# Performance work log

Measured on AMD Instinct MI355X. Metric: run time of the kernel, lower is better.

The kernel has to match this reference:

```python
import jax, jax.numpy as jnp
import numpy as np
from jax.ops import segment_sum

N = 100000   # nodes
E = 1600000  # edges
F = 128      # node feature dim
H = 128      # hidden dim
FE = 16      # edge feature dim
G = 256      # num graphs
EPS = 1e-5   # batch-norm eps


def setup_inputs() -> dict:
    key = jax.random.key(0)
    ks = jax.random.split(key, 16)
    s = 0.05
    return {
        "x": jax.random.normal(ks[0], (N, F), jnp.float32),
        "edge_index": jax.random.randint(ks[1], (2, E), 0, N, dtype=jnp.int32),
        "edge_attr": jax.random.normal(ks[2], (E, FE), jnp.float32),
        "batch_idx": jnp.sort(jax.random.randint(ks[3], (N,), 0, G, dtype=jnp.int32)),
        # GCN layer 1
        "W_g1": jax.random.normal(ks[4], (F, H), jnp.float32) * s,
        "b_g1": jnp.zeros((H,), jnp.float32),
        "gamma1": jnp.ones((H,), jnp.float32),
        "beta1": jnp.zeros((H,), jnp.float32),
        # GCN layer 2
        "W_g2": jax.random.normal(ks[5], (H, H), jnp.float32) * s,
        "b_g2": jnp.zeros((H,), jnp.float32),
        "gamma2": jnp.ones((H,), jnp.float32),
        "beta2": jnp.zeros((H,), jnp.float32),
        # edge encoder MLP
        "W_e1": jax.random.normal(ks[6], (FE, H), jnp.float32) * s,
        "b_e1": jnp.zeros((H,), jnp.float32),
        "W_e2": jax.random.normal(ks[7], (H, H), jnp.float32) * s,
        "b_e2": jnp.zeros((H,), jnp.float32),
    }


def _gcn_bn_relu(x, src, dst, W, b, gamma, beta):
    """GCNConv (sym-normalized, self-loops) + BatchNorm1d (batch stats) + ReLU."""
    h = x @ W                                             # [N, H]
    ones = jnp.ones((E,), h.dtype)
    deg = segment_sum(ones, dst, num_segments=N) + 1.0    # self-loop degree
    dinv = jax.lax.rsqrt(deg)                             # [N]
    norm = dinv[src] * dinv[dst]                          # [E]
    agg = segment_sum(h[src] * norm[:, None], dst, num_segments=N)
    out = agg + h * (dinv * dinv)[:, None] + b            # self-loop + bias
    mu = out.mean(axis=0)
    var = out.var(axis=0)
    out = (out - mu) * jax.lax.rsqrt(var + EPS) * gamma + beta
    return jax.nn.relu(out)


def reference(x, edge_index, edge_attr, batch_idx, W_g1, b_g1, gamma1, beta1,
              W_g2, b_g2, gamma2, beta2, W_e1, b_e1, W_e2, b_e2):
    src, dst = edge_index[0], edge_index[1]
    h = _gcn_bn_relu(x, src, dst, W_g1, b_g1, gamma1, beta1)
    h = _gcn_bn_relu(h, src, dst, W_g2, b_g2, gamma2, beta2)

    # global mean pool over nodes per graph
    node_cnt = segment_sum(jnp.ones((N,), h.dtype), batch_idx, num_segments=G)
    graph_repr = segment_sum(h, batch_idx, num_segments=G) / jnp.maximum(node_cnt, 1.0)[:, None]

    # edge encoder MLP + per-graph edge mean (vectorized version of the loop)
    e = jax.nn.relu(edge_attr @ W_e1 + b_e1) @ W_e2 + b_e2   # [E, H]
    edge_batch = batch_idx[src]                              # [E]
    edge_cnt = segment_sum(jnp.ones((E,), e.dtype), edge_batch, num_segments=G)
    edge_sum = segment_sum(e, edge_batch, num_segments=G)
    edge_repr = jnp.where(edge_cnt[:, None] > 0, edge_sum / jnp.maximum(edge_cnt, 1.0)[:, None], 0.0)

    return graph_repr + edge_repr  # [G, H]
```

## Files before the change

### kernel.cpp

```cpp
#include <hip/hip_runtime.h>
#include <cstdint>

__device__ inline unsigned int bfpack2(float a, float b) {
  unsigned int ua = __float_as_uint(a), ub = __float_as_uint(b);
  ua += 0x7FFFu + ((ua >> 16) & 1u);
  ub += 0x7FFFu + ((ub >> 16) & 1u);
  return (ua >> 16) | (ub & 0xFFFF0000u);
}
__device__ inline float bflo(unsigned int u) { return __uint_as_float(u << 16); }
__device__ inline float bfhi(unsigned int u) { return __uint_as_float(u & 0xFFFF0000u); }

__global__ __launch_bounds__(256) void pre_kernel(const int* __restrict__ src,
                                                  const int* __restrict__ dst,
                                                  int* __restrict__ deg,
                                                  int* __restrict__ deg2, int nE) {
  int e = blockIdx.x * 256 + threadIdx.x;
  if (e < nE) {
    atomicAdd(&deg[dst[e]], 1);
    atomicAdd(&deg2[src[e]], 1);
  }
}

__global__ __launch_bounds__(256) void dinv_kernel(const int* __restrict__ deg,
                                                   float* __restrict__ dinv, int n) {
  int i = blockIdx.x * 256 + threadIdx.x;
  if (i < n) dinv[i] = rsqrtf((float)deg[i] + 1.0f);
}

__global__ __launch_bounds__(256) void scan1_kernel(const int* __restrict__ deg,
                                                    int* __restrict__ rp,
                                                    int* __restrict__ part, int n, int pad) {
  __shared__ int sh[256];
  int b = blockIdx.x, t = threadIdx.x;
  int base = b * 1024 + t * 4;
  int v0 = (base + 0 < n) ? deg[base + 0] : 0;
  int v1 = (base + 1 < n) ? deg[base + 1] : 0;
  int v2 = (base + 2 < n) ? deg[base + 2] : 0;
  int v3 = (base + 3 < n) ? deg[base + 3] : 0;
  if (pad) {
    v0 = (v0 + 7) & ~7; v1 = (v1 + 7) & ~7;
    v2 = (v2 + 7) & ~7; v3 = (v3 + 7) & ~7;
  }
  int ts = v0 + v1 + v2 + v3;
  sh[t] = ts;
  __syncthreads();
  for (int off = 1; off < 256; off <<= 1) {
    int x = (t >= off) ? sh[t - off] : 0;
    __syncthreads();
    sh[t] += x;
    __syncthreads();
  }
  int excl = sh[t] - ts;
  if (t == 255) part[b] = sh[255];
  if (base + 0 < n) rp[base + 0] = excl;
  if (base + 1 < n) rp[base + 1] = excl + v0;
  if (base + 2 < n) rp[base + 2] = excl + v0 + v1;
  if (base + 3 < n) rp[base + 3] = excl + v0 + v1 + v2;
}

__global__ void scan2_kernel(int* part, int* rp, int nb, int n) {
  if (blockIdx.x == 0 && threadIdx.x == 0) {
    int run = 0;
    for (int i = 0; i < nb; ++i) { int v = part[i]; part[i] = run; run += v; }
    rp[n] = run;
  }
}

__global__ __launch_bounds__(256) void scan3_kernel(int* __restrict__ rp,
                                                    const int* __restrict__ part,
                                                    int* __restrict__ cursor, int n) {
  int i = blockIdx.x * 256 + threadIdx.x;
  if (i < n) {
    int v = rp[i] + part[i >> 10];
    rp[i] = v;
    cursor[i] = v;
  }
}

__global__ __launch_bounds__(256) void place_kernel(const int* __restrict__ src,
                                                    const int* __restrict__ dst,
                                                    const int* __restrict__ batch,
                                                    const float* __restrict__ dinv,
                                                    int* __restrict__ cursor,
                                                    int* __restrict__ cursor2,
                                                    int* __restrict__ ssort,
                                                    float* __restrict__ wgtv,
                                                    unsigned int* __restrict__ epk, int nE) {
  int e = blockIdx.x * 256 + threadIdx.x;
  if (e < nE) {
    int s = src[e];
    int d = dst[e];
    int p1 = atomicAdd(&cursor[d], 1);
    ssort[p1] = s;
    wgtv[p1] = dinv[s] * dinv[d];
    int g = batch[s];
    int p2 = atomicAdd(&cursor2[s], 1);
    epk[p2] = ((unsigned int)g << 21) | (unsigned int)e;
  }
}

__global__ __launch_bounds__(256) void pad_kernel(const int* __restrict__ rp,
                                                  const int* __restrict__ deg,
                                                  int* __restrict__ ssort,
                                                  float* __restrict__ wgtv, int nN) {
  int i = blockIdx.x * 256 + threadIdx.x;
  if (i < nN) {
    int b = rp[i] + deg[i], e = rp[i + 1];
    for (int k = b; k < e; ++k) { ssort[k] = i; wgtv[k] = 0.f; }
  }
}

template <bool FUSED>
__global__ __launch_bounds__(256) void gemm128_kernel(const float* __restrict__ A,
                                                      const float* __restrict__ W,
                                                      const float* __restrict__ scale,
                                                      const float* __restrict__ shift,
                                                      unsigned int* __restrict__ hpk,
                                                      int nrows) {
  extern __shared__ float lds[];
  float* Ws = lds;
  float* xs = lds + 128 * 128;
  const int t = threadIdx.x;
  for (int i = t; i < (128 * 128) / 4; i += 256)
    reinterpret_cast<float4*>(Ws)[i] = reinterpret_cast<const float4*>(W)[i];
  const int wave = t >> 6, lane = t & 63;
  for (int rb = blockIdx.x * 16; rb < nrows; rb += gridDim.x * 16) {
    int nr = min(16, nrows - rb);
    __syncthreads();
    for (int i = t; i < nr * 32; i += 256) {
      float4 v = reinterpret_cast<const float4*>(A + (size_t)rb * 128)[i];
      if (FUSED) {
        float4 sc4 = reinterpret_cast<const float4*>(scale)[i & 31];
        float4 sh4 = reinterpret_cast<const float4*>(shift)[i & 31];
        v.x = fmaxf(fmaf(v.x, sc4.x, sh4.x), 0.f);
        v.y = fmaxf(fmaf(v.y, sc4.y, sh4.y), 0.f);
        v.z = fmaxf(fmaf(v.z, sc4.z, sh4.z), 0.f);
        v.w = fmaxf(fmaf(v.w, sc4.w, sh4.w), 0.f);
      }
      reinterpret_cast<float4*>(xs)[i] = v;
    }
    __syncthreads();
    float acc[4][2] = {{0.f, 0.f}, {0.f, 0.f}, {0.f, 0.f}, {0.f, 0.f}};
    const float* xw = xs + wave * 4 * 128;
#pragma unroll 4
    for (int k = 0; k < 128; ++k) {
      float w0 = Ws[k * 128 + lane];
      float w1 = Ws[k * 128 + 64 + lane];
#pragma unroll
      for (int r = 0; r < 4; ++r) {
        float a = xw[r * 128 + k];
        acc[r][0] = fmaf(a, w0, acc[r][0]);
        acc[r][1] = fmaf(a, w1, acc[r][1]);
      }
    }
#pragma unroll
    for (int r = 0; r < 4; ++r) {
      int row = rb + wave * 4 + r;
      if (row < nrows)
        hpk[(size_t)row * 64 + lane] = bfpack2(acc[r][0], acc[r][1]);
    }
  }
}

__global__ __launch_bounds__(256) void spmm_kernel(const unsigned int* __restrict__ hpk,
                                                   const float* __restrict__ dinv,
                                                   const int* __restrict__ rp,
                                                   const int* __restrict__ srcs,
                                                   const float* __restrict__ wgtv,
                                                   const float* __restrict__ bias,
                                                   float* __restrict__ outp,
                                                   float* __restrict__ bnsum,
                                                   float* __restrict__ bnsq, int nN) {
  const int lane = threadIdx.x & 63;
  const int wid = (blockIdx.x * blockDim.x + threadIdx.x) >> 6;
  const int nw = (gridDim.x * blockDim.x) >> 6;
  float b0 = bias[lane], b1 = bias[64 + lane];
  float s0 = 0.f, s1 = 0.f, q0 = 0.f, q1 = 0.f;
  for (int n = wid; n < nN; n += nw) {
    const int beg = rp[n], end = rp[n + 1];
    float aA0 = 0.f, aA1 = 0.f, aB0 = 0.f, aB1 = 0.f;
    for (int j = beg; j < end; j += 8) {
      int4 ia = reinterpret_cast<const int4*>(srcs + j)[0];
      int4 ib = reinterpret_cast<const int4*>(srcs + j)[1];
      float4 wa = reinterpret_cast<const float4*>(wgtv + j)[0];
      float4 wb = reinterpret_cast<const float4*>(wgtv + j)[1];
      unsigned int p0 = hpk[(size_t)ia.x * 64 + lane];
      unsigned int p1 = hpk[(size_t)ia.y * 64 + lane];
      unsigned int p2 = hpk[(size_t)ia.z * 64 + lane];
      unsigned int p3 = hpk[(size_t)ia.w * 64 + lane];
      unsigned int p4 = hpk[(size_t)ib.x * 64 + lane];
      unsigned int p5 = hpk[(size_t)ib.y * 64 + lane];
      unsigned int p6 = hpk[(size_t)ib.z * 64 + lane];
      unsigned int p7 = hpk[(size_t)ib.w * 64 + lane];
      aA0 = fmaf(wa.x, bflo(p0), aA0); aA1 = fmaf(wa.x, bfhi(p0), aA1);
      aB0 = fmaf(wa.y, bflo(p1), aB0); aB1 = fmaf(wa.y, bfhi(p1), aB1);
      aA0 = fmaf(wa.z, bflo(p2), aA0); aA1 = fmaf(wa.z, bfhi(p2), aA1);
      aB0 = fmaf(wa.w, bflo(p3), aB0); aB1 = fmaf(wa.w, bfhi(p3), aB1);
      aA0 = fmaf(wb.x, bflo(p4), aA0); aA1 = fmaf(wb.x, bfhi(p4), aA1);
      aB0 = fmaf(wb.y, bflo(p5), aB0); aB1 = fmaf(wb.y, bfhi(p5), aB1);
      aA0 = fmaf(wb.z, bflo(p6), aA0); aA1 = fmaf(wb.z, bfhi(p6), aA1);
      aB0 = fmaf(wb.w, bflo(p7), aB0); aB1 = fmaf(wb.w, bfhi(p7), aB1);
    }
    float a0 = aA0 + aB0, a1 = aA1 + aB1;
    float dn = dinv[n];
    float sw = dn * dn;
    unsigned int pn = hpk[(size_t)n * 64 + lane];
    float o0 = fmaf(bflo(pn), sw, a0) + b0;
    float o1 = fmaf(bfhi(pn), sw, a1) + b1;
    outp[(size_t)n * 128 + lane] = o0;
    outp[(size_t)n * 128 + 64 + lane] = o1;
    s0 += o0; s1 += o1;
    q0 = fmaf(o0, o0, q0); q1 = fmaf(o1, o1, q1);
  }
  atomicAdd(&bnsum[lane], s0);
  atomicAdd(&bnsum[64 + lane], s1);
  atomicAdd(&bnsq[lane], q0);
  atomicAdd(&bnsq[64 + lane], q1);
}

__global__ void bnfin_kernel(const float* __restrict__ sum, const float* __restrict__ sq,
                             const float* __restrict__ gamma, const float* __restrict__ beta,
                             float* __restrict__ scale, float* __restrict__ shift,
                             float invN) {
  int c = threadIdx.x;
  float mu = sum[c] * invN;
  float var = sq[c] * invN - mu * mu;
  float sc = gamma[c] * rsqrtf(var + 1e-5f);
  scale[c] = sc;
  shift[c] = beta[c] - mu * sc;
}

__global__ __launch_bounds__(256) void pool_kernel(const float* __restrict__ h,
                                                   const int* __restrict__ batch,
                                                   const float* __restrict__ scale,
                                                   const float* __restrict__ shift,
                                                   float* __restrict__ gsum,
                                                   float* __restrict__ gcnt,
                                                   int nN, int chunk) {
  const int lane = threadIdx.x & 63;
  const int wid = (blockIdx.x * blockDim.x + threadIdx.x) >> 6;
  int beg = wid * chunk;
  if (beg >= nN) return;
  int end = min(nN, beg + chunk);
  const int c2 = 2 * lane;
  float2 sc2 = *reinterpret_cast<const float2*>(scale + c2);
  float2 sh2 = *reinterpret_cast<const float2*>(shift + c2);
  int cur = -1;
  float a0 = 0.f, a1 = 0.f, cnt = 0.f;
  for (int n = beg; n < end; ++n) {
    int g = batch[n];
    if (g != cur) {
      if (cur >= 0) {
        atomicAdd(&gsum[cur * 128 + c2], a0);
        atomicAdd(&gsum[cur * 128 + c2 + 1], a1);
        if (lane == 0) atomicAdd(&gcnt[cur], cnt);
      }
      cur = g; a0 = 0.f; a1 = 0.f; cnt = 0.f;
    }
    float2 v = *reinterpret_cast<const float2*>(h + (size_t)n * 128 + c2);
    a0 += fmaxf(fmaf(v.x, sc2.x, sh2.x), 0.f);
    a1 += fmaxf(fmaf(v.y, sc2.y, sh2.y), 0.f);
    cnt += 1.f;
  }
  if (cur >= 0) {
    atomicAdd(&gsum[cur * 128 + c2], a0);
    atomicAdd(&gsum[cur * 128 + c2 + 1], a1);
    if (lane == 0) atomicAdd(&gcnt[cur], cnt);
  }
}

__global__ __launch_bounds__(256) void edge2_kernel(const float* __restrict__ ea,
                                                    const unsigned int* __restrict__ epk,
                                                    const float* __restrict__ We1,
                                                    const float* __restrict__ be1,
                                                    float* __restrict__ esum,
                                                    float* __restrict__ ecnt,
                                                    int nE, int chunk) {
  const int lane = threadIdx.x & 63;
  const int wid = (blockIdx.x * blockDim.x + threadIdx.x) >> 6;
  int beg = wid * chunk;
  if (beg >= nE) return;
  int end = min(nE, beg + chunk);
  float w0[16], w1[16];
#pragma unroll
  for (int k = 0; k < 16; ++k) {
    w0[k] = We1[k * 128 + lane];
    w1[k] = We1[k * 128 + 64 + lane];
  }
  float b0 = be1[lane], b1 = be1[64 + lane];
  int cur = -1;
  float a0 = 0.f, a1 = 0.f, cnt = 0.f;
  for (int j = beg; j < end; ++j) {
    unsigned int pk = epk[j];
    int g = (int)(pk >> 21);
    int e = (int)(pk & 0x1FFFFFu);
    if (g != cur) {
      if (cur >= 0) {
        atomicAdd(&esum[cur * 128 + lane], a0);
        atomicAdd(&esum[cur * 128 + 64 + lane], a1);
        if (lane == 0) atomicAdd(&ecnt[cur], cnt);
      }
      cur = g; a0 = 0.f; a1 = 0.f; cnt = 0.f;
    }
    const float4* eap = reinterpret_cast<const float4*>(ea + (size_t)e * 16);
    float4 t0 = eap[0], t1 = eap[1], t2 = eap[2], t3 = eap[3];
    float u0 = b0, u1 = b1;
    u0 = fmaf(t0.x, w0[0], u0);  u1 = fmaf(t0.x, w1[0], u1);
    u0 = fmaf(t0.y, w0[1], u0);  u1 = fmaf(t0.y, w1[1], u1);
    u0 = fmaf(t0.z, w0[2], u0);  u1 = fmaf(t0.z, w1[2], u1);
    u0 = fmaf(t0.w, w0[3], u0);  u1 = fmaf(t0.w, w1[3], u1);
    u0 = fmaf(t1.x, w0[4], u0);  u1 = fmaf(t1.x, w1[4], u1);
    u0 = fmaf(t1.y, w0[5], u0);  u1 = fmaf(t1.y, w1[5], u1);
    u0 = fmaf(t1.z, w0[6], u0);  u1 = fmaf(t1.z, w1[6], u1);
    u0 = fmaf(t1.w, w0[7], u0);  u1 = fmaf(t1.w, w1[7], u1);
    u0 = fmaf(t2.x, w0[8], u0);  u1 = fmaf(t2.x, w1[8], u1);
    u0 = fmaf(t2.y, w0[9], u0);  u1 = fmaf(t2.y, w1[9], u1);
    u0 = fmaf(t2.z, w0[10], u0); u1 = fmaf(t2.z, w1[10], u1);
    u0 = fmaf(t2.w, w0[11], u0); u1 = fmaf(t2.w, w1[11], u1);
    u0 = fmaf(t3.x, w0[12], u0); u1 = fmaf(t3.x, w1[12], u1);
    u0 = fmaf(t3.y, w0[13], u0); u1 = fmaf(t3.y, w1[13], u1);
    u0 = fmaf(t3.z, w0[14], u0); u1 = fmaf(t3.z, w1[14], u1);
    u0 = fmaf(t3.w, w0[15], u0); u1 = fmaf(t3.w, w1[15], u1);
    a0 += fmaxf(u0, 0.f);
    a1 += fmaxf(u1, 0.f);
    cnt += 1.f;
  }
  if (cur >= 0) {
    atomicAdd(&esum[cur * 128 + lane], a0);
    atomicAdd(&esum[cur * 128 + 64 + lane], a1);
    if (lane == 0) atomicAdd(&ecnt[cur], cnt);
  }
}

__global__ __launch_bounds__(128) void final_kernel(const float* __restrict__ gsum,
                                                    const float* __restrict__ gcnt,
                                                    const float* __restrict__ esum,
                                                    const float* __restrict__ ecnt,
                                                    const float* __restrict__ We2,
                                                    const float* __restrict__ be2,
                                                    float* __restrict__ out) {
  __shared__ float row[128];
  int g = blockIdx.x, c = threadIdx.x;
  row[c] = esum[g * 128 + c];
  __syncthreads();
  float acc = 0.f;
#pragma unroll 4
  for (int k = 0; k < 128; ++k) acc = fmaf(row[k], We2[k * 128 + c], acc);
  float ce = ecnt[g];
  float er = (ce > 0.f) ? (acc / ce + be2[c]) : 0.f;
  float cn = gcnt[g];
  float gr = gsum[g * 128 + c] / fmaxf(cn, 1.f);
  out[g * 128 + c] = gr + er;
}

extern "C" void kernel_launch(void* const* d_in, const int* in_sizes, int n_in,
                              void* d_out, int out_size, void* d_ws, size_t ws_size,
                              hipStream_t stream) {
  const float* x    = (const float*)d_in[0];
  const int*   ei   = (const int*)d_in[1];
  const float* ea   = (const float*)d_in[2];
  const int*   bidx = (const int*)d_in[3];
  const float* Wg1  = (const float*)d_in[4];
  const float* bg1  = (const float*)d_in[5];
  const float* gm1  = (const float*)d_in[6];
  const float* bt1  = (const float*)d_in[7];
  const float* Wg2  = (const float*)d_in[8];
  const float* bg2  = (const float*)d_in[9];
  const float* gm2  = (const float*)d_in[10];
  const float* bt2  = (const float*)d_in[11];
  const float* We1  = (const float*)d_in[12];
  const float* be1  = (const float*)d_in[13];
  const float* We2  = (const float*)d_in[14];
  const float* be2  = (const float*)d_in[15];
  float* out = (float*)d_out;

  const int N = in_sizes[3];
  const int E = in_sizes[1] / 2;
  const int G = out_size / 128;
  const int* srcp = ei;
  const int* dstp = ei + E;
  const int Epad = E + 8 * N;

  char* w = (char*)d_ws;
  auto alloc = [&](size_t b) {
    char* p = w;
    w += (b + 15) & ~(size_t)15;
    return p;
  };
  float* bufB    = (float*)alloc((size_t)N * 128 * 4);
  unsigned int* hpk = (unsigned int*)alloc((size_t)N * 64 * 4);
  int*   ssort   = (int*)alloc((size_t)Epad * 4);
  float* wgtv    = (float*)alloc((size_t)Epad * 4);
  unsigned int* epk = (unsigned int*)alloc((size_t)E * 4);
  int*   rp      = (int*)alloc((size_t)(N + 1) * 4);
  int*   rp2     = (int*)alloc((size_t)(N + 1) * 4);
  int*   cursor  = (int*)alloc((size_t)N * 4);
  int*   cursor2 = (int*)alloc((size_t)N * 4);
  float* dinv    = (float*)alloc((size_t)N * 4);
  char* zbase = w;
  int*   deg  = (int*)alloc((size_t)N * 4);
  int*   deg2 = (int*)alloc((size_t)N * 4);
  float* bs1  = (float*)alloc(512);
  float* bq1  = (float*)alloc(512);
  float* bs2  = (float*)alloc(512);
  float* bq2  = (float*)alloc(512);
  float* gsum = (float*)alloc((size_t)G * 128 * 4);
  float* gcnt = (float*)alloc((size_t)G * 4);
  float* esum = (float*)alloc((size_t)G * 128 * 4);
  float* ecnt = (float*)alloc((size_t)G * 4);
  int*   part  = (int*)alloc(4096);
  int*   part2 = (int*)alloc(4096);
  size_t zbytes = (size_t)(w - zbase);
  float* sc1 = (float*)alloc(512);
  float* sh1 = (float*)alloc(512);
  float* sc2 = (float*)alloc(512);
  float* sh2 = (float*)alloc(512);

  hipMemsetAsync(zbase, 0, zbytes, stream);

  (void)hipFuncSetAttribute((const void*)gemm128_kernel<false>,
                            hipFuncAttributeMaxDynamicSharedMemorySize, 73728);
  (void)hipFuncSetAttribute((const void*)gemm128_kernel<true>,
                            hipFuncAttributeMaxDynamicSharedMemorySize, 73728);

  pre_kernel<<<(E + 255) / 256, 256, 0, stream>>>(srcp, dstp, deg, deg2, E);
  dinv_kernel<<<(N + 255) / 256, 256, 0, stream>>>(deg, dinv, N);
  int nb = (N + 1023) / 1024;
  scan1_kernel<<<nb, 256, 0, stream>>>(deg, rp, part, N, 1);
  scan2_kernel<<<1, 1, 0, stream>>>(part, rp, nb, N);
  scan3_kernel<<<(N + 255) / 256, 256, 0, stream>>>(rp, part, cursor, N);
  scan1_kernel<<<nb, 256, 0, stream>>>(deg2, rp2, part2, N, 0);
  scan2_kernel<<<1, 1, 0, stream>>>(part2, rp2, nb, N);
  scan3_kernel<<<(N + 255) / 256, 256, 0, stream>>>(rp2, part2, cursor2, N);
  place_kernel<<<(E + 255) / 256, 256, 0, stream>>>(srcp, dstp, bidx, dinv, cursor,
                                                    cursor2, ssort, wgtv, epk, E);
  pad_kernel<<<(N + 255) / 256, 256, 0, stream>>>(rp, deg, ssort, wgtv, N);

  gemm128_kernel<false><<<512, 256, 73728, stream>>>(x, Wg1, nullptr, nullptr, hpk, N);
  spmm_kernel<<<2048, 256, 0, stream>>>(hpk, dinv, rp, ssort, wgtv, bg1, bufB, bs1, bq1, N);
  bnfin_kernel<<<1, 128, 0, stream>>>(bs1, bq1, gm1, bt1, sc1, sh1, 1.0f / (float)N);

  gemm128_kernel<true><<<512, 256, 73728, stream>>>(bufB, Wg2, sc1, sh1, hpk, N);
  spmm_kernel<<<2048, 256, 0, stream>>>(hpk, dinv, rp, ssort, wgtv, bg2, bufB, bs2, bq2, N);
  bnfin_kernel<<<1, 128, 0, stream>>>(bs2, bq2, gm2, bt2, sc2, sh2, 1.0f / (float)N);

  int nwp = (2048 * 256) / 64;
  int chunkN = (N + nwp - 1) / nwp;
  pool_kernel<<<2048, 256, 0, stream>>>(bufB, bidx, sc2, sh2, gsum, gcnt, N, chunkN);
  int nwe = (2048 * 256) / 64;
  int chunkE = (E + nwe - 1) / nwe;
  edge2_kernel<<<2048, 256, 0, stream>>>(ea, epk, We1, be1, esum, ecnt, E, chunkE);
  final_kernel<<<G, 128, 0, stream>>>(gsum, gcnt, esum, ecnt, We2, be2, out);
}
```

Before: 1.527 ms.

## Merge preprocessing launches, interleave CSR index/weight, co-run edge MLP with SpMM

Collapses the two scan pipelines and the dinv computation into three combined launches, and merges placement with padding into one kernel, which cuts the number of small launches. The CSR source index and normalization weight are now stored interleaved as int2, so SpMM reads both with one stream of vector loads instead of two separate arrays. The edge-encoder reduction is moved into extra blocks of the first SpMM launch so it runs alongside the memory-bound aggregation rather than as its own pass. The trade-off is that edge blocks now compete with SpMM for compute units and bandwidth, and the edge work is split across fewer waves with larger chunks.

```diff
diff --git a/kernel.cpp b/kernel.cpp
--- a/kernel.cpp
+++ b/kernel.cpp
@@ -21,22 +21,25 @@
   }
 }
 
-__global__ __launch_bounds__(256) void dinv_kernel(const int* __restrict__ deg,
-                                                   float* __restrict__ dinv, int n) {
-  int i = blockIdx.x * 256 + threadIdx.x;
-  if (i < n) dinv[i] = rsqrtf((float)deg[i] + 1.0f);
-}
-
-__global__ __launch_bounds__(256) void scan1_kernel(const int* __restrict__ deg,
+__global__ __launch_bounds__(256) void scanA_kernel(const int* __restrict__ deg,
+                                                    const int* __restrict__ deg2,
                                                     int* __restrict__ rp,
-                                                    int* __restrict__ part, int n, int pad) {
+                                                    int* __restrict__ rp2,
+                                                    int* __restrict__ part,
+                                                    int* __restrict__ part2,
+                                                    int n, int nb) {
   __shared__ int sh[256];
   int b = blockIdx.x, t = threadIdx.x;
-  int base = b * 1024 + t * 4;
-  int v0 = (base + 0 < n) ? deg[base + 0] : 0;
-  int v1 = (base + 1 < n) ? deg[base + 1] : 0;
-  int v2 = (base + 2 < n) ? deg[base + 2] : 0;
-  int v3 = (base + 3 < n) ? deg[base + 3] : 0;
+  const int* d = (b < nb) ? deg : deg2;
+  int* r = (b < nb) ? rp : rp2;
+  int* p = (b < nb) ? part : part2;
+  int pad = (b < nb) ? 1 : 0;
+  int bb = (b < nb) ? b : b - nb;
+  int base = bb * 1024 + t * 4;
+  int v0 = (base + 0 < n) ? d[base + 0] : 0;
+  int v1 = (base + 1 < n) ? d[base + 1] : 0;
+  int v2 = (base + 2 < n) ? d[base + 2] : 0;
+  int v3 = (base + 3 < n) ? d[base + 3] : 0;
   if (pad) {
     v0 = (v0 + 7) & ~7; v1 = (v1 + 7) & ~7;
     v2 = (v2 + 7) & ~7; v3 = (v3 + 7) & ~7;
@@ -51,62 +54,71 @@
     __syncthreads();
   }
   int excl = sh[t] - ts;
-  if (t == 255) part[b] = sh[255];
-  if (base + 0 < n) rp[base + 0] = excl;
-  if (base + 1 < n) rp[base + 1] = excl + v0;
-  if (base + 2 < n) rp[base + 2] = excl + v0 + v1;
-  if (base + 3 < n) rp[base + 3] = excl + v0 + v1 + v2;
-}
-
-__global__ void scan2_kernel(int* part, int* rp, int nb, int n) {
-  if (blockIdx.x == 0 && threadIdx.x == 0) {
+  if (t == 255) p[bb] = sh[255];
+  if (base + 0 < n) r[base + 0] = excl;
+  if (base + 1 < n) r[base + 1] = excl + v0;
+  if (base + 2 < n) r[base + 2] = excl + v0 + v1;
+  if (base + 3 < n) r[base + 3] = excl + v0 + v1 + v2;
+}
+
+__global__ void scanB_kernel(int* part, int* part2, int* rp, int* rp2, int nb, int n) {
+  if (threadIdx.x == 0) {
+    int* p = (blockIdx.x == 0) ? part : part2;
+    int* r = (blockIdx.x == 0) ? rp : rp2;
     int run = 0;
-    for (int i = 0; i < nb; ++i) { int v = part[i]; part[i] = run; run += v; }
-    rp[n] = run;
-  }
-}
-
-__global__ __launch_bounds__(256) void scan3_kernel(int* __restrict__ rp,
+    for (int i = 0; i < nb; ++i) { int v = p[i]; p[i] = run; run += v; }
+    r[n] = run;
+  }
+}
+
+__global__ __launch_bounds__(256) void scanC_kernel(int* __restrict__ rp,
+                                                    int* __restrict__ rp2,
                                                     const int* __restrict__ part,
-                                                    int* __restrict__ cursor, int n) {
+                                                    const int* __restrict__ part2,
+                                                    int* __restrict__ cursor,
+                                                    int* __restrict__ cursor2,
+                                                    const int* __restrict__ deg,
+                                                    float* __restrict__ dinv, int n) {
   int i = blockIdx.x * 256 + threadIdx.x;
   if (i < n) {
     int v = rp[i] + part[i >> 10];
     rp[i] = v;
     cursor[i] = v;
-  }
-}
-
-__global__ __launch_bounds__(256) void place_kernel(const int* __restrict__ src,
-                                                    const int* __restrict__ dst,
-                                                    const int* __restrict__ batch,
-                                                    const float* __restrict__ dinv,
-                                                    int* __restrict__ cursor,
-                                                    int* __restrict__ cursor2,
-                                                    int* __restrict__ ssort,
-                                                    float* __restrict__ wgtv,
-                                                    unsigned int* __restrict__ epk, int nE) {
-  int e = blockIdx.x * 256 + threadIdx.x;
-  if (e < nE) {
-    int s = src[e];
-    int d = dst[e];
+    dinv[i] = rsqrtf((float)deg[i] + 1.0f);
+  } else if (i < 2 * n) {
+    int j = i - n;
+    int v = rp2[j] + part2[j >> 10];
+    rp2[j] = v;
+    cursor2[j] = v;
+  }
+}
+
+__global__ __launch_bounds__(256) void placepad_kernel(const int* __restrict__ src,
+                                                       const int* __restrict__ dst,
+                                                       const int* __restrict__ batch,
+                                                       const float* __restrict__ dinv,
+                                                       int* __restrict__ cursor,
+                                                       int* __restrict__ cursor2,
+                                                       int2* __restrict__ swv,
+                                                       unsigned int* __restrict__ epk,
+                                                       const int* __restrict__ rp,
+                                                       const int* __restrict__ deg,
+                                                       int nE, int nN) {
+  int t = blockIdx.x * 256 + threadIdx.x;
+  if (t < nE) {
+    int s = src[t];
+    int d = dst[t];
     int p1 = atomicAdd(&cursor[d], 1);
-    ssort[p1] = s;
-    wgtv[p1] = dinv[s] * dinv[d];
+    int2 sw; sw.x = s; sw.y = __float_as_int(dinv[s] * dinv[d]);
+    swv[p1] = sw;
     int g = batch[s];
     int p2 = atomicAdd(&cursor2[s], 1);
-    epk[p2] = ((unsigned int)g << 21) | (unsigned int)e;
-  }
-}
-
-__global__ __launch_bounds__(256) void pad_kernel(const int* __restrict__ rp,
-                                                  const int* __restrict__ deg,
-                                                  int* __restrict__ ssort,
-                                                  float* __restrict__ wgtv, int nN) {
-  int i = blockIdx.x * 256 + threadIdx.x;
-  if (i < nN) {
+    epk[p2] = ((unsigned int)g << 21) | (unsigned int)t;
+  } else if (t < nE + nN) {
+    int i = t - nE;
     int b = rp[i] + deg[i], e = rp[i + 1];
-    for (int k = b; k < e; ++k) { ssort[k] = i; wgtv[k] = 0.f; }
+    int2 z; z.x = i; z.y = 0;
+    for (int k = b; k < e; ++k) swv[k] = z;
   }
 }
 
@@ -162,44 +174,108 @@
   }
 }
 
-__global__ __launch_bounds__(256) void spmm_kernel(const unsigned int* __restrict__ hpk,
-                                                   const float* __restrict__ dinv,
-                                                   const int* __restrict__ rp,
-                                                   const int* __restrict__ srcs,
-                                                   const float* __restrict__ wgtv,
-                                                   const float* __restrict__ bias,
-                                                   float* __restrict__ outp,
-                                                   float* __restrict__ bnsum,
-                                                   float* __restrict__ bnsq, int nN) {
+__device__ __forceinline__ void edge_body(const float* __restrict__ ea,
+                                          const unsigned int* __restrict__ epk,
+                                          const float* __restrict__ We1,
+                                          const float* __restrict__ be1,
+                                          float* __restrict__ esum,
+                                          float* __restrict__ ecnt,
+                                          int nE, int chunk) {
   const int lane = threadIdx.x & 63;
-  const int wid = (blockIdx.x * blockDim.x + threadIdx.x) >> 6;
-  const int nw = (gridDim.x * blockDim.x) >> 6;
+  const int wid = (blockIdx.x * 256 + threadIdx.x) >> 6;
+  int beg = wid * chunk;
+  if (beg >= nE) return;
+  int end = min(nE, beg + chunk);
+  float w0[16], w1[16];
+#pragma unroll
+  for (int k = 0; k < 16; ++k) {
+    w0[k] = We1[k * 128 + lane];
+    w1[k] = We1[k * 128 + 64 + lane];
+  }
+  float b0 = be1[lane], b1 = be1[64 + lane];
+  int cur = -1;
+  float a0 = 0.f, a1 = 0.f, cnt = 0.f;
+  for (int j = beg; j < end; ++j) {
+    unsigned int pk = epk[j];
+    int g = (int)(pk >> 21);
+    int e = (int)(pk & 0x1FFFFFu);
+    if (g != cur) {
+      if (cur >= 0) {
+        atomicAdd(&esum[cur * 128 + lane], a0);
+        atomicAdd(&esum[cur * 128 + 64 + lane], a1);
+        if (lane == 0) atomicAdd(&ecnt[cur], cnt);
+      }
+      cur = g; a0 = 0.f; a1 = 0.f; cnt = 0.f;
+    }
+    const float4* eap = reinterpret_cast<const float4*>(ea + (size_t)e * 16);
+    float4 t0 = eap[0], t1 = eap[1], t2 = eap[2], t3 = eap[3];
+    float u0 = b0, u1 = b1;
+    u0 = fmaf(t0.x, w0[0], u0);  u1 = fmaf(t0.x, w1[0], u1);
+    u0 = fmaf(t0.y, w0[1], u0);  u1 = fmaf(t0.y, w1[1], u1);
+    u0 = fmaf(t0.z, w0[2], u0);  u1 = fmaf(t0.z, w1[2], u1);
+    u0 = fmaf(t0.w, w0[3], u0);  u1 = fmaf(t0.w, w1[3], u1);
+    u0 = fmaf(t1.x, w0[4], u0);  u1 = fmaf(t1.x, w1[4], u1);
+    u0 = fmaf(t1.y, w0[5], u0);  u1 = fmaf(t1.y, w1[5], u1);
+    u0 = fmaf(t1.z, w0[6], u0);  u1 = fmaf(t1.z, w1[6], u1);
+    u0 = fmaf(t1.w, w0[7], u0);  u1 = fmaf(t1.w, w1[7], u1);
+    u0 = fmaf(t2.x, w0[8], u0);  u1 = fmaf(t2.x, w1[8], u1);
+    u0 = fmaf(t2.y, w0[9], u0);  u1 = fmaf(t2.y, w1[9], u1);
+    u0 = fmaf(t2.z, w0[10], u0); u1 = fmaf(t2.z, w1[10], u1);
+    u0 = fmaf(t2.w, w0[11], u0); u1 = fmaf(t2.w, w1[11], u1);
+    u0 = fmaf(t3.x, w0[12], u0); u1 = fmaf(t3.x, w1[12], u1);
+    u0 = fmaf(t3.y, w0[13], u0); u1 = fmaf(t3.y, w1[13], u1);
+    u0 = fmaf(t3.z, w0[14], u0); u1 = fmaf(t3.z, w1[14], u1);
+    u0 = fmaf(t3.w, w0[15], u0); u1 = fmaf(t3.w, w1[15], u1);
+    a0 += fmaxf(u0, 0.f);
+    a1 += fmaxf(u1, 0.f);
+    cnt += 1.f;
+  }
+  if (cur >= 0) {
+    atomicAdd(&esum[cur * 128 + lane], a0);
+    atomicAdd(&esum[cur * 128 + 64 + lane], a1);
+    if (lane == 0) atomicAdd(&ecnt[cur], cnt);
+  }
+}
+
+__device__ __forceinline__ void spmm_body(const unsigned int* __restrict__ hpk,
+                                          const float* __restrict__ dinv,
+                                          const int* __restrict__ rp,
+                                          const int2* __restrict__ swv,
+                                          const float* __restrict__ bias,
+                                          float* __restrict__ outp,
+                                          float* __restrict__ bnsum,
+                                          float* __restrict__ bnsq, int nN, int eb) {
+  const int lane = threadIdx.x & 63;
+  const int wid = ((blockIdx.x - eb) * 256 + threadIdx.x) >> 6;
+  const int nw = (gridDim.x - eb) * 4;
   float b0 = bias[lane], b1 = bias[64 + lane];
   float s0 = 0.f, s1 = 0.f, q0 = 0.f, q1 = 0.f;
   for (int n = wid; n < nN; n += nw) {
     const int beg = rp[n], end = rp[n + 1];
     float aA0 = 0.f, aA1 = 0.f, aB0 = 0.f, aB1 = 0.f;
     for (int j = beg; j < end; j += 8) {
-      int4 ia = reinterpret_cast<const int4*>(srcs + j)[0];
-      int4 ib = reinterpret_cast<const int4*>(srcs + j)[1];
-      float4 wa = reinterpret_cast<const float4*>(wgtv + j)[0];
-      float4 wb = reinterpret_cast<const float4*>(wgtv + j)[1];
-      unsigned int p0 = hpk[(size_t)ia.x * 64 + lane];
-      unsigned int p1 = hpk[(size_t)ia.y * 64 + lane];
-      unsigned int p2 = hpk[(size_t)ia.z * 64 + lane];
-      unsigned int p3 = hpk[(size_t)ia.w * 64 + lane];
-      unsigned int p4 = hpk[(size_t)ib.x * 64 + lane];
-      unsigned int p5 = hpk[(size_t)ib.y * 64 + lane];
-      unsigned int p6 = hpk[(size_t)ib.z * 64 + lane];
-      unsigned int p7 = hpk[(size_t)ib.w * 64 + lane];
-      aA0 = fmaf(wa.x, bflo(p0), aA0); aA1 = fmaf(wa.x, bfhi(p0), aA1);
-      aB0 = fmaf(wa.y, bflo(p1), aB0); aB1 = fmaf(wa.y, bfhi(p1), aB1);
-      aA0 = fmaf(wa.z, bflo(p2), aA0); aA1 = fmaf(wa.z, bfhi(p2), aA1);
-      aB0 = fmaf(wa.w, bflo(p3), aB0); aB1 = fmaf(wa.w, bfhi(p3), aB1);
-      aA0 = fmaf(wb.x, bflo(p4), aA0); aA1 = fmaf(wb.x, bfhi(p4), aA1);
-      aB0 = fmaf(wb.y, bflo(p5), aB0); aB1 = fmaf(wb.y, bfhi(p5), aB1);
-      aA0 = fmaf(wb.z, bflo(p6), aA0); aA1 = fmaf(wb.z, bfhi(p6), aA1);
-      aB0 = fmaf(wb.w, bflo(p7), aB0); aB1 = fmaf(wb.w, bfhi(p7), aB1);
+      const int4* q = reinterpret_cast<const int4*>(swv + j);
+      int4 A = q[0], B = q[1], C = q[2], D = q[3];
+      unsigned int p0 = hpk[(size_t)A.x * 64 + lane];
+      unsigned int p1 = hpk[(size_t)A.z * 64 + lane];
+      unsigned int p2 = hpk[(size_t)B.x * 64 + lane];
+      unsigned int p3 = hpk[(size_t)B.z * 64 + lane];
+      unsigned int p4 = hpk[(size_t)C.x * 64 + lane];
+      unsigned int p5 = hpk[(size_t)C.z * 64 + lane];
+      unsigned int p6 = hpk[(size_t)D.x * 64 + lane];
+      unsigned int p7 = hpk[(size_t)D.z * 64 + lane];
+      float w0 = __int_as_float(A.y), w1 = __int_as_float(A.w);
+      float w2 = __int_as_float(B.y), w3 = __int_as_float(B.w);
+      float w4 = __int_as_float(C.y), w5 = __int_as_float(C.w);
+      float w6 = __int_as_float(D.y), w7 = __int_as_float(D.w);
+      aA0 = fmaf(w0, bflo(p0), aA0); aA1 = fmaf(w0, bfhi(p0), aA1);
+      aB0 = fmaf(w1, bflo(p1), aB0); aB1 = fmaf(w1, bfhi(p1), aB1);
+      aA0 = fmaf(w2, bflo(p2), aA0); aA1 = fmaf(w2, bfhi(p2), aA1);
+      aB0 = fmaf(w3, bflo(p3), aB0); aB1 = fmaf(w3, bfhi(p3), aB1);
+      aA0 = fmaf(w4, bflo(p4), aA0); aA1 = fmaf(w4, bfhi(p4), aA1);
+      aB0 = fmaf(w5, bflo(p5), aB0); aB1 = fmaf(w5, bfhi(p5), aB1);
+      aA0 = fmaf(w6, bflo(p6), aA0); aA1 = fmaf(w6, bfhi(p6), aA1);
+      aB0 = fmaf(w7, bflo(p7), aB0); aB1 = fmaf(w7, bfhi(p7), aB1);
     }
     float a0 = aA0 + aB0, a1 = aA1 + aB1;
     float dn = dinv[n];
@@ -216,6 +292,28 @@
   atomicAdd(&bnsum[64 + lane], s1);
   atomicAdd(&bnsq[lane], q0);
   atomicAdd(&bnsq[64 + lane], q1);
+}
+
+__global__ __launch_bounds__(256) void spmm_edge_kernel(const unsigned int* __restrict__ hpk,
+                                                        const float* __restrict__ dinv,
+                                                        const int* __restrict__ rp,
+                                                        const int2* __restrict__ swv,
+                                                        const float* __restrict__ bias,
+                                                        float* __restrict__ outp,
+                                                        float* __restrict__ bnsum,
+                                                        float* __restrict__ bnsq, int nN,
+                                                        const float* __restrict__ ea,
+                                                        const unsigned int* __restrict__ epk,
+                                                        const float* __restrict__ We1,
+                                                        const float* __restrict__ be1,
+                                                        float* __restrict__ esum,
+                                                        float* __restrict__ ecnt,
+                                                        int nE, int chunkE, int eb) {
+  if ((int)blockIdx.x < eb) {
+    edge_body(ea, epk, We1, be1, esum, ecnt, nE, chunkE);
+  } else {
+    spmm_body(hpk, dinv, rp, swv, bias, outp, bnsum, bnsq, nN, eb);
+  }
 }
 
 __global__ void bnfin_kernel(const float* __restrict__ sum, const float* __restrict__ sq,
@@ -269,69 +367,6 @@
   }
 }
 
-__global__ __launch_bounds__(256) void edge2_kernel(const float* __restrict__ ea,
-                                                    const unsigned int* __restrict__ epk,
-                                                    const float* __restrict__ We1,
-                                                    const float* __restrict__ be1,
-                                                    float* __restrict__ esum,
-                                                    float* __restrict__ ecnt,
-                                                    int nE, int chunk) {
-  const int lane = threadIdx.x & 63;
-  const int wid = (blockIdx.x * blockDim.x + threadIdx.x) >> 6;
-  int beg = wid * chunk;
-  if (beg >= nE) return;
-  int end = min(nE, beg + chunk);
-  float w0[16], w1[16];
-#pragma unroll
-  for (int k = 0; k < 16; ++k) {
-    w0[k] = We1[k * 128 + lane];
-    w1[k] = We1[k * 128 + 64 + lane];
-  }
-  float b0 = be1[lane], b1 = be1[64 + lane];
-  int cur = -1;
-  float a0 = 0.f, a1 = 0.f, cnt = 0.f;
-  for (int j = beg; j < end; ++j) {
-    unsigned int pk = epk[j];
-    int g = (int)(pk >> 21);
-    int e = (int)(pk & 0x1FFFFFu);
-    if (g != cur) {
-      if (cur >= 0) {
-        atomicAdd(&esum[cur * 128 + lane], a0);
-        atomicAdd(&esum[cur * 128 + 64 + lane], a1);
-        if (lane == 0) atomicAdd(&ecnt[cur], cnt);
-      }
-      cur = g; a0 = 0.f; a1 = 0.f; cnt = 0.f;
-    }
-    const float4* eap = reinterpret_cast<const float4*>(ea + (size_t)e * 16);
-    float4 t0 = eap[0], t1 = eap[1], t2 = eap[2], t3 = eap[3];
-    float u0 = b0, u1 = b1;
-    u0 = fmaf(t0.x, w0[0], u0);  u1 = fmaf(t0.x, w1[0], u1);
-    u0 = fmaf(t0.y, w0[1], u0);  u1 = fmaf(t0.y, w1[1], u1);
-    u0 = fmaf(t0.z, w0[2], u0);  u1 = fmaf(t0.z, w1[2], u1);
-    u0 = fmaf(t0.w, w0[3], u0);  u1 = fmaf(t0.w, w1[3], u1);
-    u0 = fmaf(t1.x, w0[4], u0);  u1 = fmaf(t1.x, w1[4], u1);
-    u0 = fmaf(t1.y, w0[5], u0);  u1 = fmaf(t1.y, w1[5], u1);
-    u0 = fmaf(t1.z, w0[6], u0);  u1 = fmaf(t1.z, w1[6], u1);
-    u0 = fmaf(t1.w, w0[7], u0);  u1 = fmaf(t1.w, w1[7], u1);
-    u0 = fmaf(t2.x, w0[8], u0);  u1 = fmaf(t2.x, w1[8], u1);
-    u0 = fmaf(t2.y, w0[9], u0);  u1 = fmaf(t2.y, w1[9], u1);
-    u0 = fmaf(t2.z, w0[10], u0); u1 = fmaf(t2.z, w1[10], u1);
-    u0 = fmaf(t2.w, w0[11], u0); u1 = fmaf(t2.w, w1[11], u1);
-    u0 = fmaf(t3.x, w0[12], u0); u1 = fmaf(t3.x, w1[12], u1);
-    u0 = fmaf(t3.y, w0[13], u0); u1 = fmaf(t3.y, w1[13], u1);
-    u0 = fmaf(t3.z, w0[14], u0); u1 = fmaf(t3.z, w1[14], u1);
-    u0 = fmaf(t3.w, w0[15], u0); u1 = fmaf(t3.w, w1[15], u1);
-    a0 += fmaxf(u0, 0.f);
-    a1 += fmaxf(u1, 0.f);
-    cnt += 1.f;
-  }
-  if (cur >= 0) {
-    atomicAdd(&esum[cur * 128 + lane], a0);
-    atomicAdd(&esum[cur * 128 + 64 + lane], a1);
-    if (lane == 0) atomicAdd(&ecnt[cur], cnt);
-  }
-}
-
 __global__ __launch_bounds__(128) void final_kernel(const float* __restrict__ gsum,
                                                     const float* __restrict__ gcnt,
                                                     const float* __restrict__ esum,
@@ -389,8 +424,7 @@
   };
   float* bufB    = (float*)alloc((size_t)N * 128 * 4);
   unsigned int* hpk = (unsigned int*)alloc((size_t)N * 64 * 4);
-  int*   ssort   = (int*)alloc((size_t)Epad * 4);
-  float* wgtv    = (float*)alloc((size_t)Epad * 4);
+  int2*  swv     = (int2*)alloc((size_t)Epad * 8);
   unsigned int* epk = (unsigned int*)alloc((size_t)E * 4);
   int*   rp      = (int*)alloc((size_t)(N + 1) * 4);
   int*   rp2     = (int*)alloc((size_t)(N + 1) * 4);
@@ -424,31 +458,30 @@
                             hipFuncAttributeMaxDynamicSharedMemorySize, 73728);
 
   pre_kernel<<<(E + 255) / 256, 256, 0, stream>>>(srcp, dstp, deg, deg2, E);
-  dinv_kernel<<<(N + 255) / 256, 256, 0, stream>>>(deg, dinv, N);
   int nb = (N + 1023) / 1024;
-  scan1_kernel<<<nb, 256, 0, stream>>>(deg, rp, part, N, 1);
-  scan2_kernel<<<1, 1, 0, stream>>>(part, rp, nb, N);
-  scan3_kernel<<<(N + 255) / 256, 256, 0, stream>>>(rp, part, cursor, N);
-  scan1_kernel<<<nb, 256, 0, stream>>>(deg2, rp2, part2, N, 0);
-  scan2_kernel<<<1, 1, 0, stream>>>(part2, rp2, nb, N);
-  scan3_kernel<<<(N + 255) / 256, 256, 0, stream>>>(rp2, part2, cursor2, N);
-  place_kernel<<<(E + 255) / 256, 256, 0, stream>>>(srcp, dstp, bidx, dinv, cursor,
-                                                    cursor2, ssort, wgtv, epk, E);
-  pad_kernel<<<(N + 255) / 256, 256, 0, stream>>>(rp, deg, ssort, wgtv, N);
+  scanA_kernel<<<2 * nb, 256, 0, stream>>>(deg, deg2, rp, rp2, part, part2, N, nb);
+  scanB_kernel<<<2, 64, 0, stream>>>(part, part2, rp, rp2, nb, N);
+  scanC_kernel<<<(2 * N + 255) / 256, 256, 0, stream>>>(rp, rp2, part, part2, cursor,
+                                                        cursor2, deg, dinv, N);
+  placepad_kernel<<<(E + N + 255) / 256, 256, 0, stream>>>(srcp, dstp, bidx, dinv, cursor,
+                                                           cursor2, swv, epk, rp, deg, E, N);
+
+  const int EB = 512;
+  int nwe = EB * 4;
+  int chunkE = (E + nwe - 1) / nwe;
 
   gemm128_kernel<false><<<512, 256, 73728, stream>>>(x, Wg1, nullptr, nullptr, hpk, N);
-  spmm_kernel<<<2048, 256, 0, stream>>>(hpk, dinv, rp, ssort, wgtv, bg1, bufB, bs1, bq1, N);
+  spmm_edge_kernel<<<EB + 2048, 256, 0, stream>>>(hpk, dinv, rp, swv, bg1, bufB, bs1, bq1, N,
+                                                  ea, epk, We1, be1, esum, ecnt, E, chunkE, EB);
   bnfin_kernel<<<1, 128, 0, stream>>>(bs1, bq1, gm1, bt1, sc1, sh1, 1.0f / (float)N);
 
   gemm128_kernel<true><<<512, 256, 73728, stream>>>(bufB, Wg2, sc1, sh1, hpk, N);
-  spmm_kernel<<<2048, 256, 0, stream>>>(hpk, dinv, rp, ssort, wgtv, bg2, bufB, bs2, bq2, N);
+  spmm_edge_kernel<<<2048, 256, 0, stream>>>(hpk, dinv, rp, swv, bg2, bufB, bs2, bq2, N,
+                                             ea, epk, We1, be1, esum, ecnt, 0, 1, 0);
   bnfin_kernel<<<1, 128, 0, stream>>>(bs2, bq2, gm2, bt2, sc2, sh2, 1.0f / (float)N);
 
   int nwp = (2048 * 256) / 64;
   int chunkN = (N + nwp - 1) / nwp;
   pool_kernel<<<2048, 256, 0, stream>>>(bufB, bidx, sc2, sh2, gsum, gcnt, N, chunkN);
-  int nwe = (2048 * 256) / 64;
-  int chunkE = (E + nwe - 1) / nwe;
-  edge2_kernel<<<2048, 256, 0, stream>>>(ea, epk, We1, be1, esum, ecnt, E, chunkE);
   final_kernel<<<G, 128, 0, stream>>>(gsum, gcnt, esum, ecnt, We2, be2, out);
 }
```

Result: slower. 1.737 ms (+13.7%).
